# Optimization experiments

Measured on AMD Instinct MI355X. Metric: run time of the kernel, lower is better.

Reference implementation:

```python
import jax, jax.numpy as jnp
import numpy as np

B, N, DIM, H = 2, 4096, 1024, 16
LAT = 1024
CTX = N - LAT            # 3072 context tokens
SEG = 12                 # num_segments
CHUNK = CTX // SEG       # 256 tokens per segment
D = DIM // H             # 64 head dim
SCALE = D ** -0.5
LN_EPS = 1e-5
NEG = float(-np.finfo(np.float32).max)


def _split_heads(t):  # [B, N, DIM] -> [(B*H), N, D]
    return t.reshape(B, N, H, D).transpose(0, 2, 1, 3).reshape(B * H, N, D)


def _merge_heads(t):  # [(B*H), n, D] -> [B, n, DIM]
    n = t.shape[1]
    return t.reshape(B, H, n, D).transpose(0, 2, 1, 3).reshape(B, n, DIM)


def _layernorm(t, g, b):  # LN over last dim (head dim)
    mu = t.mean(-1, keepdims=True)
    var = ((t - mu) ** 2).mean(-1, keepdims=True)
    return (t - mu) * jax.lax.rsqrt(var + LN_EPS) * g + b


def _rope(t):  # rotary embedding over full head dim, half-split rotate
    pos = jnp.arange(N, dtype=jnp.float32)
    inv = 1.0 / (10000.0 ** (jnp.arange(0, D, 2, dtype=jnp.float32) / D))
    freqs = pos[:, None] * inv[None, :]          # [N, D/2]
    emb = jnp.concatenate([freqs, freqs], -1)    # [N, D]
    cos, sin = jnp.cos(emb), jnp.sin(emb)
    rot = jnp.concatenate([-t[..., D // 2:], t[..., : D // 2]], -1)
    return t * cos + rot * sin


def setup_inputs() -> dict:
    key = jax.random.key(0)
    ks = jax.random.split(key, 4)
    s = 0.02
    return {
        "x": jax.random.normal(ks[0], (B, N, DIM), jnp.float32),
        "Wq": jax.random.normal(ks[1], (DIM, DIM), jnp.float32) * s,
        "Wkv": jax.random.normal(ks[2], (DIM, DIM), jnp.float32) * s,
        "Wo": jax.random.normal(ks[3], (DIM, DIM), jnp.float32) * s,
        "bo": jnp.zeros((DIM,), jnp.float32),
        "ln_g": jnp.ones((D,), jnp.float32),
        "ln_b": jnp.zeros((D,), jnp.float32),
    }


def reference(x, Wq, Wkv, Wo, bo, ln_g, ln_b):
    q = _split_heads(x @ Wq)    # [(BH), N, D]
    kv = _split_heads(x @ Wkv)  # [(BH), N, D]
    q, kv = _rope(q), _rope(kv)

    lkv = _layernorm(kv, ln_g, ln_b)  # normalized keys/values, full seq

    q_lat = q[:, CTX:] * SCALE                                   # [(BH), LAT, D]
    q_ctx = (q[:, :CTX] * SCALE).reshape(B * H, SEG, CHUNK, D)   # segmented ctx queries
    lkv_ctx = lkv[:, :CTX].reshape(B * H, SEG, CHUNK, D)         # segmented norm'd kv

    # latent queries: full attention over all N positions, causal among latents
    lsim = jnp.einsum('bid,bjd->bij', q_lat, lkv)                # [(BH), LAT, N]
    tri = jnp.triu(jnp.ones((LAT, LAT), bool), 1)
    lat_block = jnp.where(tri, NEG, lsim[:, :, CTX:])
    lsim = jnp.concatenate([lsim[:, :, :CTX], lat_block], axis=-1)
    attn = jax.nn.softmax(lsim, axis=-1)
    out_lat = jnp.einsum('bij,bjd->bid', attn, lkv)              # [(BH), LAT, D]

    # context queries: block-diagonal segmented local attention (non-causal)
    sim_ctx = jnp.einsum('bsid,bsjd->bsij', q_ctx, lkv_ctx)      # [(BH), SEG, CHUNK, CHUNK]
    attn_ctx = jax.nn.softmax(sim_ctx, axis=-1)
    out_ctx = jnp.einsum('bsij,bsjd->bsid', attn_ctx, lkv_ctx).reshape(B * H, CTX, D)

    out = jnp.concatenate([_merge_heads(out_ctx), _merge_heads(out_lat)], axis=1)
    return out @ Wo + bo
```

## Files before the change

### kernel.cpp

```cpp
#include <hip/hip_runtime.h>
#include <math.h>

#define NB_B 2
#define NB_N 4096
#define NB_DIM 1024
#define NB_H 16
#define NB_D 64
#define NB_CTX 3072
#define NSPLIT 4
#define QSCALE 0.18033688011112042f
#define NEGF -3.0e38f

typedef __attribute__((ext_vector_type(8))) short short8;
typedef __attribute__((ext_vector_type(4))) short s4v;
typedef __attribute__((ext_vector_type(4))) float f32x4;

#if __has_builtin(__builtin_amdgcn_mfma_f32_16x16x16bf16_1k)
__device__ __forceinline__ f32x4 mfma16(s4v a, s4v b, f32x4 c) {
  return __builtin_amdgcn_mfma_f32_16x16x16bf16_1k(a, b, c, 0, 0, 0);
}
#else
__device__ __forceinline__ f32x4 mfma16(s4v a, s4v b, f32x4 c) {
  f32x4 d;
  asm volatile("v_mfma_f32_16x16x16_bf16 %0, %1, %2, %3"
               : "=v"(d) : "v"(a), "v"(b), "v"(c));
  return d;
}
#endif

__device__ __forceinline__ unsigned short f2bf(float f) {
  union { float f; unsigned u; } v; v.f = f;
  unsigned r = v.u + 0x7fffu + ((v.u >> 16) & 1u);
  return (unsigned short)(r >> 16);
}

__device__ __forceinline__ void async16(const void* g, void* l) {
  typedef const unsigned int __attribute__((address_space(1)))* gas_t;
  typedef unsigned int __attribute__((address_space(3)))* las_t;
  __builtin_amdgcn_global_load_lds((gas_t)(unsigned long long)g,
                                   (las_t)(unsigned)(unsigned long long)l,
                                   16, 0, 0);
}

__global__ __launch_bounds__(256) void k_prep(
    const float* __restrict__ x,
    const float* __restrict__ Wq, const float* __restrict__ Wkv, const float* __restrict__ Wo,
    unsigned short* __restrict__ xb, unsigned short* __restrict__ WqkvT,
    unsigned short* __restrict__ WoT, float2* __restrict__ tab)
{
  __shared__ float tile[64][65];
  const int bx = blockIdx.x, tid = threadIdx.x;
  if (bx < 2048) {
    const float4* x4 = (const float4*)x;
    ushort4* xb4 = (ushort4*)xb;
    const int n4 = (NB_B * NB_N * NB_DIM) / 4;
    for (int i = bx * 256 + tid; i < n4; i += 2048 * 256) {
      float4 v = x4[i];
      ushort4 o;
      o.x = f2bf(v.x); o.y = f2bf(v.y); o.z = f2bf(v.z); o.w = f2bf(v.w);
      xb4[i] = o;
    }
  } else if (bx < 2816) {
    int idx = bx - 2048;
    int z = idx >> 8, rem = idx & 255;
    const float* W; unsigned short* out;
    if (z == 0)      { W = Wq;  out = WqkvT; }
    else if (z == 1) { W = Wkv; out = WqkvT + 1024 * 1024; }
    else             { W = Wo;  out = WoT; }
    int c0 = (rem & 15) * 64, k0 = (rem >> 4) * 64;
    int tx = tid & 63, ty = tid >> 6;
    #pragma unroll
    for (int i = 0; i < 16; ++i) {
      int k = ty + i * 4;
      tile[k][tx] = W[(long)(k0 + k) * 1024 + c0 + tx];
    }
    __syncthreads();
    #pragma unroll
    for (int i = 0; i < 16; ++i) {
      int c = ty + i * 4;
      out[(long)(c0 + c) * 1024 + k0 + tx] = f2bf(tile[tx][c]);
    }
  } else {
    int idx = (bx - 2816) * 256 + tid;
    int n = idx >> 5, fi = idx & 31;
    float inv = exp2f(-(float)fi * (13.287712379549449f / 32.0f));
    float ang = (float)n * inv;
    float s, c;
    sincosf(ang, &s, &c);
    tab[idx] = make_float2(c, s);
  }
}

__global__ __launch_bounds__(256) void k_gemm_qkv(
    const unsigned short* __restrict__ A,
    const unsigned short* __restrict__ Bt,
    unsigned short* __restrict__ qf,
    unsigned short* __restrict__ lkvp,
    const float2* __restrict__ tab,
    const float* __restrict__ ln_g,
    const float* __restrict__ ln_b)
{
  __shared__ unsigned short As[128 * 32];
  __shared__ unsigned short Bs[128 * 32];
  const int tid = threadIdx.x;
  const int w = tid >> 6, lane = tid & 63;
  const int wr = w >> 1, wc = w & 1;
  const int quad = lane >> 4, l15 = lane & 15;
  const long tm = (long)blockIdx.y * 128, tn = (long)blockIdx.x * 128;
  const int K = 1024;

  f32x4 acc[4][4];
  #pragma unroll
  for (int i = 0; i < 4; ++i)
    #pragma unroll
    for (int j = 0; j < 4; ++j)
      acc[i][j] = (f32x4){0.f, 0.f, 0.f, 0.f};

  const unsigned short* Ag0 = A + (tm + w * 16 + (lane >> 2)) * K + (lane & 3) * 8;
  const unsigned short* Bg0 = Bt + (tn + w * 16 + (lane >> 2)) * K + (lane & 3) * 8;
  const unsigned short* Ag1 = Ag0 + (long)64 * K;
  const unsigned short* Bg1 = Bg0 + (long)64 * K;
  unsigned short* Al0 = &As[(w * 16) * 32];
  unsigned short* Al1 = &As[(64 + w * 16) * 32];
  unsigned short* Bl0 = &Bs[(w * 16) * 32];
  unsigned short* Bl1 = &Bs[(64 + w * 16) * 32];

  for (int k0 = 0; k0 < K; k0 += 32) {
    __syncthreads();
    async16(Ag0 + k0, Al0);
    async16(Ag1 + k0, Al1);
    async16(Bg0 + k0, Bl0);
    async16(Bg1 + k0, Bl1);
    __syncthreads();
    short8 af[4], bfr[4];
    #pragma unroll
    for (int i = 0; i < 4; ++i)
      af[i] = *(const short8*)&As[(wr * 64 + i * 16 + l15) * 32 + quad * 8];
    #pragma unroll
    for (int j = 0; j < 4; ++j)
      bfr[j] = *(const short8*)&Bs[(wc * 64 + j * 16 + l15) * 32 + quad * 8];
    #pragma unroll
    for (int i = 0; i < 4; ++i)
      #pragma unroll
      for (int j = 0; j < 4; ++j)
        acc[i][j] = __builtin_amdgcn_mfma_f32_16x16x32_bf16(af[i], bfr[j], acc[i][j], 0, 0, 0);
  }

  const int col_base = (int)tn + wc * 64;
  const bool is_q = col_base < 1024;
  const int hh = (col_base & 1023) >> 6;
  unsigned short* dst = is_q ? qf : lkvp;
  float g_ln[4], b_ln[4];
  #pragma unroll
  for (int j = 0; j < 4; ++j) { g_ln[j] = ln_g[j * 16 + l15]; b_ln[j] = ln_b[j * 16 + l15]; }

  const int row_base = (int)tm + wr * 64;
  #pragma unroll
  for (int i = 0; i < 4; ++i) {
    #pragma unroll
    for (int r = 0; r < 4; ++r) {
      const int row = row_base + i * 16 + quad * 4 + r;
      const int n = row & 4095, b = row >> 12;
      const float2 cs0 = tab[n * 32 + l15];
      const float2 cs1 = tab[n * 32 + 16 + l15];
      float val[4];
      #pragma unroll
      for (int j = 0; j < 4; ++j) {
        float t = acc[i][j][r], pt = acc[i][j ^ 2][r];
        float2 cs = (j & 1) ? cs1 : cs0;
        float rot = (j < 2) ? -pt : pt;
        val[j] = t * cs.x + rot * cs.y;
      }
      unsigned short* orow = dst + ((long)(b * 16 + hh) * NB_N + n) * 64;
      if (is_q) {
        #pragma unroll
        for (int j = 0; j < 4; ++j)
          orow[j * 16 + l15] = f2bf(val[j] * QSCALE);
      } else {
        float s = val[0] + val[1] + val[2] + val[3];
        #pragma unroll
        for (int o = 1; o < 16; o <<= 1) s += __shfl_xor(s, o);
        const float mu = s * 0.015625f;
        float dv[4], vs = 0.f;
        #pragma unroll
        for (int j = 0; j < 4; ++j) { dv[j] = val[j] - mu; vs += dv[j] * dv[j]; }
        #pragma unroll
        for (int o = 1; o < 16; o <<= 1) vs += __shfl_xor(vs, o);
        const float rr = rsqrtf(vs * 0.015625f + 1e-5f);
        #pragma unroll
        for (int j = 0; j < 4; ++j)
          orow[j * 16 + l15] = f2bf(dv[j] * rr * g_ln[j] + b_ln[j]);
      }
    }
  }
}

__global__ __launch_bounds__(256) void k_gemm_bt(
    const unsigned short* __restrict__ A,
    const unsigned short* __restrict__ Bt,
    float* __restrict__ C,
    const float* __restrict__ bias,
    int K, int ldc)
{
  __shared__ unsigned short As[128 * 32];
  __shared__ unsigned short Bs[128 * 32];
  const int tid = threadIdx.x;
  const int w = tid >> 6, lane = tid & 63;
  const int wr = w >> 1, wc = w & 1;
  const int quad = lane >> 4, l15 = lane & 15;
  const long tm = (long)blockIdx.y * 128, tn = (long)blockIdx.x * 128;

  f32x4 acc[4][4];
  #pragma unroll
  for (int i = 0; i < 4; ++i)
    #pragma unroll
    for (int j = 0; j < 4; ++j)
      acc[i][j] = (f32x4){0.f, 0.f, 0.f, 0.f};

  const unsigned short* Ag0 = A + (tm + w * 16 + (lane >> 2)) * K + (lane & 3) * 8;
  const unsigned short* Bg0 = Bt + (tn + w * 16 + (lane >> 2)) * K + (lane & 3) * 8;
  const unsigned short* Ag1 = Ag0 + (long)64 * K;
  const unsigned short* Bg1 = Bg0 + (long)64 * K;
  unsigned short* Al0 = &As[(w * 16) * 32];
  unsigned short* Al1 = &As[(64 + w * 16) * 32];
  unsigned short* Bl0 = &Bs[(w * 16) * 32];
  unsigned short* Bl1 = &Bs[(64 + w * 16) * 32];

  for (int k0 = 0; k0 < K; k0 += 32) {
    __syncthreads();
    async16(Ag0 + k0, Al0);
    async16(Ag1 + k0, Al1);
    async16(Bg0 + k0, Bl0);
    async16(Bg1 + k0, Bl1);
    __syncthreads();
    short8 af[4], bfr[4];
    #pragma unroll
    for (int i = 0; i < 4; ++i)
      af[i] = *(const short8*)&As[(wr * 64 + i * 16 + l15) * 32 + quad * 8];
    #pragma unroll
    for (int j = 0; j < 4; ++j)
      bfr[j] = *(const short8*)&Bs[(wc * 64 + j * 16 + l15) * 32 + quad * 8];
    #pragma unroll
    for (int i = 0; i < 4; ++i)
      #pragma unroll
      for (int j = 0; j < 4; ++j)
        acc[i][j] = __builtin_amdgcn_mfma_f32_16x16x32_bf16(af[i], bfr[j], acc[i][j], 0, 0, 0);
  }

  #pragma unroll
  for (int j = 0; j < 4; ++j) {
    const long col = tn + wc * 64 + j * 16 + l15;
    const float bv = bias ? bias[col] : 0.0f;
    #pragma unroll
    for (int i = 0; i < 4; ++i) {
      #pragma unroll
      for (int r = 0; r < 4; ++r) {
        const long row = tm + wr * 64 + i * 16 + quad * 4 + r;
        C[row * ldc + col] = acc[i][j][r] + bv;
      }
    }
  }
}

__global__ __launch_bounds__(256) void k_attn(
    const unsigned short* __restrict__ qf,
    const unsigned short* __restrict__ lkv,
    unsigned short* __restrict__ attn_out,
    float* __restrict__ Opart,
    float* __restrict__ mpart,
    float* __restrict__ lpart)
{
  __shared__ unsigned short smem[18432];

  const int tid = threadIdx.x;
  const int w = tid >> 6, lane = tid & 63;
  const int quad = lane >> 4, l15 = lane & 15;

  const int bx = blockIdx.x;
  int bh, q0tok, kstart, kt0, kt1, q0lat, s6 = 0, qb = 0;
  bool latent;
  if (bx < 256 * NSPLIT) {
    latent = true;
    qb = bx / NSPLIT;
    s6 = bx % NSPLIT;
    bh = qb >> 3;
    q0lat = (qb & 7) * 128;
    q0tok = NB_CTX + q0lat;
    kstart = 0;
    int nkt = (NB_CTX + q0lat + 128) >> 6;
    kt0 = (s6 * nkt) / NSPLIT;
    kt1 = ((s6 + 1) * nkt) / NSPLIT;
  } else {
    latent = false;
    int idx = bx - 256 * NSPLIT;
    bh = idx / 24;
    int r2 = idx % 24;
    int seg = r2 >> 1;
    q0lat = 0;
    q0tok = seg * 256 + (r2 & 1) * 128;
    kstart = seg * 256;
    kt0 = 0; kt1 = 4;
  }

  const unsigned short* qbase = qf + ((long)bh * NB_N + q0tok) * 64;
  const unsigned short* kbase = lkv + (long)bh * NB_N * 64;

  short8 qfr[2][2];
  #pragma unroll
  for (int qg = 0; qg < 2; ++qg)
    #pragma unroll
    for (int kc = 0; kc < 2; ++kc)
      qfr[qg][kc] = *(const short8*)(qbase + (w * 32 + qg * 16 + l15) * 64 + kc * 32 + quad * 8);

  const int kp = tid >> 3, sdc = tid & 7;

  uint4 gA, gB;
  {
    const int key0 = kstart + kt0 * 64;
    gA = *(const uint4*)(kbase + (long)(key0 + 2 * kp) * 64 + sdc * 8);
    gB = *(const uint4*)(kbase + (long)(key0 + 2 * kp + 1) * 64 + sdc * 8);
  }

  {
    unsigned short* Ks0 = smem;
    unsigned short* Vt0 = smem + 4608;
    *(uint4*)&Ks0[(2 * kp) * 72 + sdc * 8] = gA;
    *(uint4*)&Ks0[(2 * kp + 1) * 72 + sdc * 8] = gB;
    const unsigned int* wA = (const unsigned int*)&gA;
    const unsigned int* wB = (const unsigned int*)&gB;
    #pragma unroll
    for (int jw = 0; jw < 4; ++jw) {
      const unsigned int lo = __builtin_amdgcn_perm(wB[jw], wA[jw], 0x05040100u);
      const unsigned int hi = __builtin_amdgcn_perm(wB[jw], wA[jw], 0x07060302u);
      const int d0 = sdc * 8 + jw * 2;
      const int xo = (2 * kp) ^ (d0 & 56);
      *(unsigned int*)&Vt0[d0 * 72 + xo] = lo;
      *(unsigned int*)&Vt0[(d0 + 1) * 72 + xo] = hi;
    }
  }
  if (kt0 + 1 < kt1) {
    const int key0n = kstart + (kt0 + 1) * 64;
    gA = *(const uint4*)(kbase + (long)(key0n + 2 * kp) * 64 + sdc * 8);
    gB = *(const uint4*)(kbase + (long)(key0n + 2 * kp + 1) * 64 + sdc * 8);
  }

  f32x4 ot[2][4];
  float mi[2], li[2];
  #pragma unroll
  for (int qg = 0; qg < 2; ++qg) {
    #pragma unroll
    for (int dt = 0; dt < 4; ++dt) ot[qg][dt] = (f32x4){0.f, 0.f, 0.f, 0.f};
    mi[qg] = 0.f; li[qg] = 0.f;
  }

  int cur = 0;
  for (int kt = kt0; kt < kt1; ++kt) {
    const int key0 = kstart + kt * 64;
    __syncthreads();
    const unsigned short* Ks = smem + cur;
    const unsigned short* Vt = smem + cur + 4608;

    if (kt + 1 < kt1) {
      unsigned short* Ksn = smem + (cur ^ 9216);
      unsigned short* Vtn = Ksn + 4608;
      *(uint4*)&Ksn[(2 * kp) * 72 + sdc * 8] = gA;
      *(uint4*)&Ksn[(2 * kp + 1) * 72 + sdc * 8] = gB;
      const unsigned int* wA = (const unsigned int*)&gA;
      const unsigned int* wB = (const unsigned int*)&gB;
      #pragma unroll
      for (int jw = 0; jw < 4; ++jw) {
        const unsigned int lo = __builtin_amdgcn_perm(wB[jw], wA[jw], 0x05040100u);
        const unsigned int hi = __builtin_amdgcn_perm(wB[jw], wA[jw], 0x07060302u);
        const int d0 = sdc * 8 + jw * 2;
        const int xo = (2 * kp) ^ (d0 & 56);
        *(unsigned int*)&Vtn[d0 * 72 + xo] = lo;
        *(unsigned int*)&Vtn[(d0 + 1) * 72 + xo] = hi;
      }
      if (kt + 2 < kt1) {
        const int key0n = key0 + 128;
        gA = *(const uint4*)(kbase + (long)(key0n + 2 * kp) * 64 + sdc * 8);
        gB = *(const uint4*)(kbase + (long)(key0n + 2 * kp + 1) * 64 + sdc * 8);
      }
    }

    f32x4 st[2][4];
    #pragma unroll
    for (int qg = 0; qg < 2; ++qg)
      #pragma unroll
      for (int k4 = 0; k4 < 4; ++k4)
        st[qg][k4] = (f32x4){0.f, 0.f, 0.f, 0.f};
    #pragma unroll
    for (int kc = 0; kc < 2; ++kc) {
      short8 kf[4];
      #pragma unroll
      for (int k4 = 0; k4 < 4; ++k4)
        kf[k4] = *(const short8*)&Ks[(k4 * 16 + l15) * 72 + kc * 32 + quad * 8];
      #pragma unroll
      for (int qg = 0; qg < 2; ++qg)
        #pragma unroll
        for (int k4 = 0; k4 < 4; ++k4)
          st[qg][k4] = __builtin_amdgcn_mfma_f32_16x16x32_bf16(kf[k4], qfr[qg][kc], st[qg][k4], 0, 0, 0);
    }

    if (latent && key0 + 63 >= NB_CTX) {
      #pragma unroll
      for (int qg = 0; qg < 2; ++qg) {
        const int qrow = q0lat + w * 32 + qg * 16 + l15;
        #pragma unroll
        for (int k4 = 0; k4 < 4; ++k4)
          #pragma unroll
          for (int r = 0; r < 4; ++r) {
            const int kl = key0 + k4 * 16 + quad * 4 + r - NB_CTX;
            if (kl > qrow) st[qg][k4][r] = NEGF;
          }
      }
    }

    unsigned int pk[2][4][2];
    float tmx[2], trs[2];
    #pragma unroll
    for (int qg = 0; qg < 2; ++qg) {
      float rs = 0.f;
      float mx = NEGF;
      #pragma unroll
      for (int k4 = 0; k4 < 4; ++k4) {
        unsigned int b[4];
        #pragma unroll
        for (int r = 0; r < 4; ++r) {
          float p = __builtin_amdgcn_exp2f(st[qg][k4][r] - mi[qg]);
          unsigned int pb = __float_as_uint(p) & 0xffff0000u;
          rs += __uint_as_float(pb);
          b[r] = pb;
        }
        mx = fmaxf(mx, fmaxf(fmaxf(st[qg][k4][0], st[qg][k4][1]),
                             fmaxf(st[qg][k4][2], st[qg][k4][3])));
        pk[qg][k4][0] = __builtin_amdgcn_perm(b[1], b[0], 0x07060302);
        pk[qg][k4][1] = __builtin_amdgcn_perm(b[3], b[2], 0x07060302);
      }
      tmx[qg] = mx; trs[qg] = rs;
    }

    #pragma unroll
    for (int k4 = 0; k4 < 4; ++k4) {
      s4v vf[4];
      const int kb = k4 * 16 + quad * 4;
      #pragma unroll
      for (int dt = 0; dt < 4; ++dt) {
        const int row = dt * 16 + l15;
        vf[dt] = *(const s4v*)&Vt[row * 72 + (kb ^ (row & 56))];
      }
      #pragma unroll
      for (int qg = 0; qg < 2; ++qg) {
        s4v pf;
        ((unsigned int*)&pf)[0] = pk[qg][k4][0];
        ((unsigned int*)&pf)[1] = pk[qg][k4][1];
        #pragma unroll
        for (int dt = 0; dt < 4; ++dt)
          ot[qg][dt] = mfma16(vf[dt], pf, ot[qg][dt]);
      }
    }

    #pragma unroll
    for (int qg = 0; qg < 2; ++qg) {
      float rs = trs[qg];
      rs += __shfl_xor(rs, 16);
      rs += __shfl_xor(rs, 32);
      float mx = tmx[qg];
      mx = fmaxf(mx, __shfl_xor(mx, 16));
      mx = fmaxf(mx, __shfl_xor(mx, 32));
      if (__builtin_expect(mx > mi[qg] + 8.f, 0)) {
        const float c = __builtin_amdgcn_exp2f(mi[qg] - mx);
        mi[qg] = mx;
        li[qg] = (li[qg] + rs) * c;
        #pragma unroll
        for (int dt = 0; dt < 4; ++dt) {
          ot[qg][dt][0] *= c; ot[qg][dt][1] *= c;
          ot[qg][dt][2] *= c; ot[qg][dt][3] *= c;
        }
      } else {
        li[qg] += rs;
      }
    }

    cur ^= 9216;
  }

  __syncthreads();
  if (latent) {
    const long pb = (long)(s6 * 256 + qb);
    if (quad == 0) {
      #pragma unroll
      for (int qg = 0; qg < 2; ++qg) {
        mpart[pb * 128 + w * 32 + qg * 16 + l15] = mi[qg];
        lpart[pb * 128 + w * 32 + qg * 16 + l15] = li[qg];
      }
    }
    float* obase = Opart + pb * 8192;
    #pragma unroll
    for (int qg = 0; qg < 2; ++qg) {
      const int q = w * 32 + qg * 16 + l15;
      #pragma unroll
      for (int dt = 0; dt < 4; ++dt)
        #pragma unroll
        for (int r = 0; r < 4; ++r)
          obase[(dt * 16 + quad * 4 + r) * 128 + q] = ot[qg][dt][r];
    }
  } else {
    #pragma unroll
    for (int qg = 0; qg < 2; ++qg) {
      const float inv = 1.0f / li[qg];
      const int q = w * 32 + qg * 16 + l15;
      #pragma unroll
      for (int dt = 0; dt < 4; ++dt)
        #pragma unroll
        for (int r = 0; r < 4; ++r)
          smem[q * 72 + dt * 16 + quad * 4 + r] = f2bf(ot[qg][dt][r] * inv);
    }
    __syncthreads();
    const int qrow = tid >> 1, half = tid & 1;
    const int b_ = bh >> 4, h_ = bh & 15;
    unsigned short* orow = attn_out + ((long)b_ * NB_N + q0tok + qrow) * NB_DIM + h_ * 64 + half * 32;
    #pragma unroll
    for (int v = 0; v < 4; ++v)
      *(uint4*)(orow + v * 8) = *(const uint4*)&smem[qrow * 72 + half * 32 + v * 8];
  }
}

__global__ __launch_bounds__(256) void k_combine(
    const float* __restrict__ Opart, const float* __restrict__ mpart,
    const float* __restrict__ lpart, unsigned short* __restrict__ attn_out)
{
  __shared__ unsigned short lds[9216];
  const int qb = blockIdx.x;
  const int bh = qb >> 3, qt = qb & 7;
  const int b = bh >> 4, h = bh & 15;
  const int t = threadIdx.x;
  const int qq = t & 31;
  const int dg = t >> 5;

  float m[NSPLIT][4], l[NSPLIT][4];
  float mstar[4];
  #pragma unroll
  for (int qi = 0; qi < 4; ++qi) mstar[qi] = NEGF;
  #pragma unroll
  for (int s = 0; s < NSPLIT; ++s) {
    #pragma unroll
    for (int qi = 0; qi < 4; ++qi) {
      m[s][qi] = mpart[(s * 256 + qb) * 128 + qq * 4 + qi];
      l[s][qi] = lpart[(s * 256 + qb) * 128 + qq * 4 + qi];
      mstar[qi] = fmaxf(mstar[qi], m[s][qi]);
    }
  }
  float inv[4];
  #pragma unroll
  for (int qi = 0; qi < 4; ++qi) {
    float lsum = 0.f;
    #pragma unroll
    for (int s = 0; s < NSPLIT; ++s)
      lsum += __builtin_amdgcn_exp2f(m[s][qi] - mstar[qi]) * l[s][qi];
    inv[qi] = 1.0f / lsum;
  }

  float o[8][4];
  #pragma unroll
  for (int dd = 0; dd < 8; ++dd)
    #pragma unroll
    for (int qi = 0; qi < 4; ++qi) o[dd][qi] = 0.f;
  #pragma unroll
  for (int s = 0; s < NSPLIT; ++s) {
    float wgt[4];
    #pragma unroll
    for (int qi = 0; qi < 4; ++qi)
      wgt[qi] = __builtin_amdgcn_exp2f(m[s][qi] - mstar[qi]);
    const float* base = Opart + (long)(s * 256 + qb) * 8192;
    #pragma unroll
    for (int dd = 0; dd < 8; ++dd) {
      float4 v = *(const float4*)(base + (dg * 8 + dd) * 128 + qq * 4);
      o[dd][0] += wgt[0] * v.x; o[dd][1] += wgt[1] * v.y;
      o[dd][2] += wgt[2] * v.z; o[dd][3] += wgt[3] * v.w;
    }
  }
  #pragma unroll
  for (int qi = 0; qi < 4; ++qi) {
    ushort4 u0, u1;
    u0.x = f2bf(o[0][qi] * inv[qi]); u0.y = f2bf(o[1][qi] * inv[qi]);
    u0.z = f2bf(o[2][qi] * inv[qi]); u0.w = f2bf(o[3][qi] * inv[qi]);
    u1.x = f2bf(o[4][qi] * inv[qi]); u1.y = f2bf(o[5][qi] * inv[qi]);
    u1.z = f2bf(o[6][qi] * inv[qi]); u1.w = f2bf(o[7][qi] * inv[qi]);
    *(ushort4*)&lds[(qq * 4 + qi) * 72 + dg * 8] = u0;
    *(ushort4*)&lds[(qq * 4 + qi) * 72 + dg * 8 + 4] = u1;
  }
  __syncthreads();
  const int qrow = t >> 1, half = t & 1;
  unsigned short* orow = attn_out + ((long)b * NB_N + NB_CTX + qt * 128 + qrow) * NB_DIM + h * 64 + half * 32;
  #pragma unroll
  for (int v = 0; v < 4; ++v)
    *(uint4*)(orow + v * 8) = *(const uint4*)&lds[qrow * 72 + half * 32 + v * 8];
}

extern "C" void kernel_launch(void* const* d_in, const int* in_sizes, int n_in,
                              void* d_out, int out_size, void* d_ws, size_t ws_size,
                              hipStream_t stream)
{
  const float* x    = (const float*)d_in[0];
  const float* Wq   = (const float*)d_in[1];
  const float* Wkv  = (const float*)d_in[2];
  const float* Wo   = (const float*)d_in[3];
  const float* bo   = (const float*)d_in[4];
  const float* ln_g = (const float*)d_in[5];
  const float* ln_b = (const float*)d_in[6];
  float* out = (float*)d_out;

  char* ws = (char*)d_ws;
  unsigned short* xb    = (unsigned short*)(ws);
  unsigned short* WqkvT = (unsigned short*)(ws + (size_t)(16 << 20));
  unsigned short* WoT   = (unsigned short*)(ws + (size_t)(20 << 20));
  float2*         tab   = (float2*)        (ws + (size_t)(22 << 20));
  unsigned short* qfb   = (unsigned short*)(ws + (size_t)(24 << 20));
  unsigned short* lkv   = (unsigned short*)(ws + (size_t)(40 << 20));
  unsigned short* aout  = (unsigned short*)(ws + (size_t)(56 << 20));
  float*          Opart = (float*)         (ws + (size_t)(72 << 20));
  float*          mpart = (float*)         (ws + (size_t)(112 << 20));
  float*          lpart = (float*)         (ws + (size_t)(113 << 20));

  hipLaunchKernelGGL(k_prep, dim3(3328), dim3(256), 0, stream,
                     x, Wq, Wkv, Wo, xb, WqkvT, WoT, tab);
  hipLaunchKernelGGL(k_gemm_qkv, dim3(16, 64), dim3(256), 0, stream,
                     xb, WqkvT, qfb, lkv, tab, ln_g, ln_b);
  hipLaunchKernelGGL(k_attn, dim3(256 * NSPLIT + 768), dim3(256), 0, stream,
                     qfb, lkv, aout, Opart, mpart, lpart);
  hipLaunchKernelGGL(k_combine, dim3(256), dim3(256), 0, stream,
                     Opart, mpart, lpart, aout);
  hipLaunchKernelGGL(k_gemm_bt, dim3(8, 64), dim3(256), 0, stream,
                     aout, WoT, out, bo, 1024, 1024);
}
```

Measured before the change: 282.6 us.

## Rework attention softmax with per-wave max, MFMA row sums, and unrolled double buffer

After: 266.1 us. -5.8%, faster.

```diff
diff --git a/kernel.cpp b/kernel.cpp
--- a/kernel.cpp
+++ b/kernel.cpp
@@ -32,6 +32,12 @@
   union { float f; unsigned u; } v; v.f = f;
   unsigned r = v.u + 0x7fffu + ((v.u >> 16) & 1u);
   return (unsigned short)(r >> 16);
+}
+
+__device__ __forceinline__ unsigned int cvtpk(float a, float b) {
+  unsigned int r;
+  asm("v_cvt_pk_bf16_f32 %0, %1, %2" : "=v"(r) : "v"(a), "v"(b));
+  return r;
 }
 
 __device__ __forceinline__ void async16(const void* g, void* l) {
@@ -262,6 +268,147 @@
   }
 }
 
+
+__device__ __forceinline__ void stage_kv(
+    unsigned short* __restrict__ Ksn, unsigned short* __restrict__ Vtn,
+    const int kp, const int sdc, const uint4& gA, const uint4& gB)
+{
+  *(uint4*)&Ksn[(2 * kp) * 72 + sdc * 8] = gA;
+  *(uint4*)&Ksn[(2 * kp + 1) * 72 + sdc * 8] = gB;
+  const unsigned int* wA = (const unsigned int*)&gA;
+  const unsigned int* wB = (const unsigned int*)&gB;
+  #pragma unroll
+  for (int jw = 0; jw < 4; ++jw) {
+    const unsigned int lo = __builtin_amdgcn_perm(wB[jw], wA[jw], 0x05040100u);
+    const unsigned int hi = __builtin_amdgcn_perm(wB[jw], wA[jw], 0x07060302u);
+    const int d0 = sdc * 8 + jw * 2;
+    const int xo = (2 * kp) ^ (d0 & 56);
+    *(unsigned int*)&Vtn[d0 * 72 + xo] = lo;
+    *(unsigned int*)&Vtn[(d0 + 1) * 72 + xo] = hi;
+  }
+}
+
+#define NB_PACK(QG, SUB)                                               \
+  _Pragma("unroll")                                                    \
+  for (int k4 = 0; k4 < 4; ++k4) {                                     \
+    const float p0 = __builtin_amdgcn_exp2f(st[QG][k4][0] SUB);        \
+    const float p1 = __builtin_amdgcn_exp2f(st[QG][k4][1] SUB);        \
+    const float p2 = __builtin_amdgcn_exp2f(st[QG][k4][2] SUB);        \
+    const float p3 = __builtin_amdgcn_exp2f(st[QG][k4][3] SUB);        \
+    pk[QG][k4][0] = cvtpk(p0, p1);                                     \
+    pk[QG][k4][1] = cvtpk(p2, p3);                                     \
+  }
+
+__device__ __forceinline__ void attn_tile(
+    const unsigned short* __restrict__ Ks, const unsigned short* __restrict__ Vt,
+    unsigned short* __restrict__ Ksn, unsigned short* __restrict__ Vtn,
+    const int kt, const int kt1, const int kstart, const bool latent, const int q0lat,
+    const int w, const int quad, const int l15, const int kp, const int sdc,
+    const unsigned short* __restrict__ kbase,
+    uint4& gA, uint4& gB, const short8 (&qfr)[2][2],
+    f32x4 (&ot)[2][4], f32x4 (&lacc)[2], float& miu, float& thr)
+{
+  const int key0 = kstart + kt * 64;
+  __syncthreads();
+
+  if (kt + 1 < kt1) {
+    stage_kv(Ksn, Vtn, kp, sdc, gA, gB);
+    if (kt + 2 < kt1) {
+      const long k2 = (long)(key0 + 128);
+      gA = *(const uint4*)(kbase + (k2 + 2 * kp) * 64 + sdc * 8);
+      gB = *(const uint4*)(kbase + (k2 + 2 * kp + 1) * 64 + sdc * 8);
+    }
+  }
+
+  f32x4 st[2][4];
+  #pragma unroll
+  for (int qg = 0; qg < 2; ++qg)
+    #pragma unroll
+    for (int k4 = 0; k4 < 4; ++k4)
+      st[qg][k4] = (f32x4){0.f, 0.f, 0.f, 0.f};
+  #pragma unroll
+  for (int kc = 0; kc < 2; ++kc) {
+    short8 kf[4];
+    #pragma unroll
+    for (int k4 = 0; k4 < 4; ++k4)
+      kf[k4] = *(const short8*)&Ks[(k4 * 16 + l15) * 72 + kc * 32 + quad * 8];
+    #pragma unroll
+    for (int qg = 0; qg < 2; ++qg)
+      #pragma unroll
+      for (int k4 = 0; k4 < 4; ++k4)
+        st[qg][k4] = __builtin_amdgcn_mfma_f32_16x16x32_bf16(kf[k4], qfr[qg][kc], st[qg][k4], 0, 0, 0);
+  }
+
+  if (latent && key0 + 63 >= NB_CTX) {
+    #pragma unroll
+    for (int qg = 0; qg < 2; ++qg) {
+      const int qrow = q0lat + w * 32 + qg * 16 + l15;
+      #pragma unroll
+      for (int k4 = 0; k4 < 4; ++k4)
+        #pragma unroll
+        for (int r = 0; r < 4; ++r) {
+          const int kl = key0 + k4 * 16 + quad * 4 + r - NB_CTX;
+          if (kl > qrow) st[qg][k4][r] = NEGF;
+        }
+    }
+  }
+
+  float mx = st[0][0][0];
+  #pragma unroll
+  for (int qg = 0; qg < 2; ++qg)
+    #pragma unroll
+    for (int k4 = 0; k4 < 4; ++k4)
+      mx = fmaxf(mx, fmaxf(fmaxf(st[qg][k4][0], st[qg][k4][1]),
+                           fmaxf(st[qg][k4][2], st[qg][k4][3])));
+
+  unsigned int pk[2][4][2];
+  if (miu == 0.f) {
+    NB_PACK(0, )
+    NB_PACK(1, )
+  } else {
+    NB_PACK(0, - miu)
+    NB_PACK(1, - miu)
+  }
+
+  const s4v vones = { (short)0x3F80, (short)0x3F80, (short)0x3F80, (short)0x3F80 };
+  #pragma unroll
+  for (int k4 = 0; k4 < 4; ++k4) {
+    s4v vf[4];
+    const int kb = k4 * 16 + quad * 4;
+    #pragma unroll
+    for (int dt = 0; dt < 4; ++dt) {
+      const int row = dt * 16 + l15;
+      vf[dt] = *(const s4v*)&Vt[row * 72 + (kb ^ (row & 56))];
+    }
+    #pragma unroll
+    for (int qg = 0; qg < 2; ++qg) {
+      s4v pf;
+      ((unsigned int*)&pf)[0] = pk[qg][k4][0];
+      ((unsigned int*)&pf)[1] = pk[qg][k4][1];
+      lacc[qg] = mfma16(vones, pf, lacc[qg]);
+      #pragma unroll
+      for (int dt = 0; dt < 4; ++dt)
+        ot[qg][dt] = mfma16(vf[dt], pf, ot[qg][dt]);
+    }
+  }
+
+  if (__builtin_expect(__any(mx > thr), 0)) {
+    #pragma unroll
+    for (int o = 1; o < 64; o <<= 1) mx = fmaxf(mx, __shfl_xor(mx, o));
+    const float c = __builtin_amdgcn_exp2f(miu - mx);
+    miu = mx; thr = mx + 8.f;
+    #pragma unroll
+    for (int qg = 0; qg < 2; ++qg) {
+      lacc[qg][0] *= c; lacc[qg][1] *= c; lacc[qg][2] *= c; lacc[qg][3] *= c;
+      #pragma unroll
+      for (int dt = 0; dt < 4; ++dt) {
+        ot[qg][dt][0] *= c; ot[qg][dt][1] *= c;
+        ot[qg][dt][2] *= c; ot[qg][dt][3] *= c;
+      }
+    }
+  }
+}
+
 __global__ __launch_bounds__(256) void k_attn(
     const unsigned short* __restrict__ qf,
     const unsigned short* __restrict__ lkv,
@@ -271,6 +418,10 @@
     float* __restrict__ lpart)
 {
   __shared__ unsigned short smem[18432];
+  unsigned short* const Ks0 = smem;
+  unsigned short* const Vt0 = smem + 4608;
+  unsigned short* const Ks1 = smem + 9216;
+  unsigned short* const Vt1 = smem + 13824;
 
   const int tid = threadIdx.x;
   const int w = tid >> 6, lane = tid & 63;
@@ -287,9 +438,10 @@
     q0lat = (qb & 7) * 128;
     q0tok = NB_CTX + q0lat;
     kstart = 0;
-    int nkt = (NB_CTX + q0lat + 128) >> 6;
-    kt0 = (s6 * nkt) / NSPLIT;
-    kt1 = ((s6 + 1) * nkt) / NSPLIT;
+    const int nkt = (NB_CTX + q0lat + 128) >> 6;
+    const int hk = nkt >> 1;
+    kt0 = 2 * ((s6 * hk) / NSPLIT);
+    kt1 = 2 * (((s6 + 1) * hk) / NSPLIT);
   } else {
     latent = false;
     int idx = bx - 256 * NSPLIT;
@@ -320,169 +472,28 @@
     gA = *(const uint4*)(kbase + (long)(key0 + 2 * kp) * 64 + sdc * 8);
     gB = *(const uint4*)(kbase + (long)(key0 + 2 * kp + 1) * 64 + sdc * 8);
   }
-
+  stage_kv(Ks0, Vt0, kp, sdc, gA, gB);
   {
-    unsigned short* Ks0 = smem;
-    unsigned short* Vt0 = smem + 4608;
-    *(uint4*)&Ks0[(2 * kp) * 72 + sdc * 8] = gA;
-    *(uint4*)&Ks0[(2 * kp + 1) * 72 + sdc * 8] = gB;
-    const unsigned int* wA = (const unsigned int*)&gA;
-    const unsigned int* wB = (const unsigned int*)&gB;
-    #pragma unroll
-    for (int jw = 0; jw < 4; ++jw) {
-      const unsigned int lo = __builtin_amdgcn_perm(wB[jw], wA[jw], 0x05040100u);
-      const unsigned int hi = __builtin_amdgcn_perm(wB[jw], wA[jw], 0x07060302u);
-      const int d0 = sdc * 8 + jw * 2;
-      const int xo = (2 * kp) ^ (d0 & 56);
-      *(unsigned int*)&Vt0[d0 * 72 + xo] = lo;
-      *(unsigned int*)&Vt0[(d0 + 1) * 72 + xo] = hi;
-    }
-  }
-  if (kt0 + 1 < kt1) {
-    const int key0n = kstart + (kt0 + 1) * 64;
-    gA = *(const uint4*)(kbase + (long)(key0n + 2 * kp) * 64 + sdc * 8);
-    gB = *(const uint4*)(kbase + (long)(key0n + 2 * kp + 1) * 64 + sdc * 8);
+    const int key1 = kstart + (kt0 + 1) * 64;
+    gA = *(const uint4*)(kbase + (long)(key1 + 2 * kp) * 64 + sdc * 8);
+    gB = *(const uint4*)(kbase + (long)(key1 + 2 * kp + 1) * 64 + sdc * 8);
   }
 
   f32x4 ot[2][4];
-  float mi[2], li[2];
+  f32x4 lacc[2];
+  float miu = 0.f, thr = 8.f;
   #pragma unroll
   for (int qg = 0; qg < 2; ++qg) {
     #pragma unroll
     for (int dt = 0; dt < 4; ++dt) ot[qg][dt] = (f32x4){0.f, 0.f, 0.f, 0.f};
-    mi[qg] = 0.f; li[qg] = 0.f;
-  }
-
-  int cur = 0;
-  for (int kt = kt0; kt < kt1; ++kt) {
-    const int key0 = kstart + kt * 64;
-    __syncthreads();
-    const unsigned short* Ks = smem + cur;
-    const unsigned short* Vt = smem + cur + 4608;
-
-    if (kt + 1 < kt1) {
-      unsigned short* Ksn = smem + (cur ^ 9216);
-      unsigned short* Vtn = Ksn + 4608;
-      *(uint4*)&Ksn[(2 * kp) * 72 + sdc * 8] = gA;
-      *(uint4*)&Ksn[(2 * kp + 1) * 72 + sdc * 8] = gB;
-      const unsigned int* wA = (const unsigned int*)&gA;
-      const unsigned int* wB = (const unsigned int*)&gB;
-      #pragma unroll
-      for (int jw = 0; jw < 4; ++jw) {
-        const unsigned int lo = __builtin_amdgcn_perm(wB[jw], wA[jw], 0x05040100u);
-        const unsigned int hi = __builtin_amdgcn_perm(wB[jw], wA[jw], 0x07060302u);
-        const int d0 = sdc * 8 + jw * 2;
-        const int xo = (2 * kp) ^ (d0 & 56);
-        *(unsigned int*)&Vtn[d0 * 72 + xo] = lo;
-        *(unsigned int*)&Vtn[(d0 + 1) * 72 + xo] = hi;
-      }
-      if (kt + 2 < kt1) {
-        const int key0n = key0 + 128;
-        gA = *(const uint4*)(kbase + (long)(key0n + 2 * kp) * 64 + sdc * 8);
-        gB = *(const uint4*)(kbase + (long)(key0n + 2 * kp + 1) * 64 + sdc * 8);
-      }
-    }
-
-    f32x4 st[2][4];
-    #pragma unroll
-    for (int qg = 0; qg < 2; ++qg)
-      #pragma unroll
-      for (int k4 = 0; k4 < 4; ++k4)
-        st[qg][k4] = (f32x4){0.f, 0.f, 0.f, 0.f};
-    #pragma unroll
-    for (int kc = 0; kc < 2; ++kc) {
-      short8 kf[4];
-      #pragma unroll
-      for (int k4 = 0; k4 < 4; ++k4)
-        kf[k4] = *(const short8*)&Ks[(k4 * 16 + l15) * 72 + kc * 32 + quad * 8];
-      #pragma unroll
-      for (int qg = 0; qg < 2; ++qg)
-        #pragma unroll
-        for (int k4 = 0; k4 < 4; ++k4)
-          st[qg][k4] = __builtin_amdgcn_mfma_f32_16x16x32_bf16(kf[k4], qfr[qg][kc], st[qg][k4], 0, 0, 0);
-    }
-
-    if (latent && key0 + 63 >= NB_CTX) {
-      #pragma unroll
-      for (int qg = 0; qg < 2; ++qg) {
-        const int qrow = q0lat + w * 32 + qg * 16 + l15;
-        #pragma unroll
-        for (int k4 = 0; k4 < 4; ++k4)
-          #pragma unroll
-          for (int r = 0; r < 4; ++r) {
-            const int kl = key0 + k4 * 16 + quad * 4 + r - NB_CTX;
-            if (kl > qrow) st[qg][k4][r] = NEGF;
-          }
-      }
-    }
-
-    unsigned int pk[2][4][2];
-    float tmx[2], trs[2];
-    #pragma unroll
-    for (int qg = 0; qg < 2; ++qg) {
-      float rs = 0.f;
-      float mx = NEGF;
-      #pragma unroll
-      for (int k4 = 0; k4 < 4; ++k4) {
-        unsigned int b[4];
-        #pragma unroll
-        for (int r = 0; r < 4; ++r) {
-          float p = __builtin_amdgcn_exp2f(st[qg][k4][r] - mi[qg]);
-          unsigned int pb = __float_as_uint(p) & 0xffff0000u;
-          rs += __uint_as_float(pb);
-          b[r] = pb;
-        }
-        mx = fmaxf(mx, fmaxf(fmaxf(st[qg][k4][0], st[qg][k4][1]),
-                             fmaxf(st[qg][k4][2], st[qg][k4][3])));
-        pk[qg][k4][0] = __builtin_amdgcn_perm(b[1], b[0], 0x07060302);
-        pk[qg][k4][1] = __builtin_amdgcn_perm(b[3], b[2], 0x07060302);
-      }
-      tmx[qg] = mx; trs[qg] = rs;
-    }
-
-    #pragma unroll
-    for (int k4 = 0; k4 < 4; ++k4) {
-      s4v vf[4];
-      const int kb = k4 * 16 + quad * 4;
-      #pragma unroll
-      for (int dt = 0; dt < 4; ++dt) {
-        const int row = dt * 16 + l15;
-        vf[dt] = *(const s4v*)&Vt[row * 72 + (kb ^ (row & 56))];
-      }
-      #pragma unroll
-      for (int qg = 0; qg < 2; ++qg) {
-        s4v pf;
-        ((unsigned int*)&pf)[0] = pk[qg][k4][0];
-        ((unsigned int*)&pf)[1] = pk[qg][k4][1];
-        #pragma unroll
-        for (int dt = 0; dt < 4; ++dt)
-          ot[qg][dt] = mfma16(vf[dt], pf, ot[qg][dt]);
-      }
-    }
-
-    #pragma unroll
-    for (int qg = 0; qg < 2; ++qg) {
-      float rs = trs[qg];
-      rs += __shfl_xor(rs, 16);
-      rs += __shfl_xor(rs, 32);
-      float mx = tmx[qg];
-      mx = fmaxf(mx, __shfl_xor(mx, 16));
-      mx = fmaxf(mx, __shfl_xor(mx, 32));
-      if (__builtin_expect(mx > mi[qg] + 8.f, 0)) {
-        const float c = __builtin_amdgcn_exp2f(mi[qg] - mx);
-        mi[qg] = mx;
-        li[qg] = (li[qg] + rs) * c;
-        #pragma unroll
-        for (int dt = 0; dt < 4; ++dt) {
-          ot[qg][dt][0] *= c; ot[qg][dt][1] *= c;
-          ot[qg][dt][2] *= c; ot[qg][dt][3] *= c;
-        }
-      } else {
-        li[qg] += rs;
-      }
-    }
-
-    cur ^= 9216;
+    lacc[qg] = (f32x4){0.f, 0.f, 0.f, 0.f};
+  }
+
+  for (int kt = kt0; kt < kt1; kt += 2) {
+    attn_tile(Ks0, Vt0, Ks1, Vt1, kt,     kt1, kstart, latent, q0lat,
+              w, quad, l15, kp, sdc, kbase, gA, gB, qfr, ot, lacc, miu, thr);
+    attn_tile(Ks1, Vt1, Ks0, Vt0, kt + 1, kt1, kstart, latent, q0lat,
+              w, quad, l15, kp, sdc, kbase, gA, gB, qfr, ot, lacc, miu, thr);
   }
 
   __syncthreads();
@@ -491,8 +502,8 @@
     if (quad == 0) {
       #pragma unroll
       for (int qg = 0; qg < 2; ++qg) {
-        mpart[pb * 128 + w * 32 + qg * 16 + l15] = mi[qg];
-        lpart[pb * 128 + w * 32 + qg * 16 + l15] = li[qg];
+        mpart[pb * 128 + w * 32 + qg * 16 + l15] = miu;
+        lpart[pb * 128 + w * 32 + qg * 16 + l15] = lacc[qg][0];
       }
     }
     float* obase = Opart + pb * 8192;
@@ -508,7 +519,7 @@
   } else {
     #pragma unroll
     for (int qg = 0; qg < 2; ++qg) {
-      const float inv = 1.0f / li[qg];
+      const float inv = 1.0f / lacc[qg][0];
       const int q = w * 32 + qg * 16 + l15;
       #pragma unroll
       for (int dt = 0; dt < 4; ++dt)
```
